# Performance work log

Measured on AMD Instinct MI355X. Metric: run time of the kernel, lower is better.

The kernel has to match this reference:

```python
import jax, jax.numpy as jnp
import numpy as np

T, N = 1024, 1024
DT = 0.5          # timestep used for velocity
DIS_THRESH = 12.0 # neighbor inclusion radius


def setup_inputs() -> dict:
    key = jax.random.key(0)
    ks = jax.random.split(key, 13)
    inp = {"a": jax.random.normal(ks[0], (T, N, 2), dtype=jnp.float32) * 10.0}
    # shared MLP (single linear layer) parameters
    inp["W1"] = jax.random.normal(ks[1], (1, 2), dtype=jnp.float32) * 0.5
    inp["b1"] = jax.random.normal(ks[2], (1,), dtype=jnp.float32) * 0.1
    inp["W2"] = jax.random.normal(ks[3], (1, 2), dtype=jnp.float32) * 0.5
    inp["b2"] = jax.random.normal(ks[4], (1,), dtype=jnp.float32) * 0.1
    inp["W3"] = jax.random.normal(ks[5], (1, 2), dtype=jnp.float32) * 0.5
    inp["b3"] = jax.random.normal(ks[6], (1,), dtype=jnp.float32) * 0.1
    inp["W4"] = jax.random.normal(ks[7], (1, 2), dtype=jnp.float32) * 0.5
    inp["b4"] = jax.random.normal(ks[8], (1,), dtype=jnp.float32) * 0.1
    inp["W5"] = jax.random.normal(ks[9], (1, 4), dtype=jnp.float32) * 0.5
    inp["b5"] = jax.random.normal(ks[10], (1,), dtype=jnp.float32) * 0.1
    inp["W6"] = jax.random.normal(ks[11], (64, 4), dtype=jnp.float32) * 0.5
    inp["b6"] = jax.random.normal(ks[12], (64,), dtype=jnp.float32) * 0.1
    return inp


def reference(a, W1, b1, W2, b2, W3, b3, W4, b4, W5, b5, W6, b6):
    # a: [T, N, 2]. Effective computation per (t in 1..T-1, node i),
    # neighbor j = N-1 (the inner qqq loop only keeps its last iteration).
    p = a[1:]              # [T-1, N, 2] current positions
    prev = a[:-1]          # [T-1, N, 2] previous positions
    pj = p[:, -1:, :]      # [T-1, 1, 2] neighbor (last node)

    dis = jnp.sqrt(jnp.sum((p - pj) ** 2, axis=-1))      # [T-1, N]
    d = p - prev                                          # displacement
    v = jnp.sqrt(jnp.sum(d ** 2, axis=-1)) / DT           # [T-1, N]
    ang = jnp.arctan2(d[..., 1], d[..., 0])               # [T-1, N]

    v_j = v[:, -1:]       # [T-1, 1]
    ang_j = ang[:, -1:]   # [T-1, 1]
    mask = (dis <= DIS_THRESH).astype(a.dtype)            # [T-1, N]

    def lin2(W, b, x0, x1):
        # 2-input linear; neighbor term masked out when dis > thresh
        return W[0, 0] * x0 + W[0, 1] * x1 + b[0]

    x_m = lin2(W1, b1, p[..., 0], mask * pj[..., 0])
    y_m = lin2(W2, b2, p[..., 1], mask * pj[..., 1])
    v_m = lin2(W3, b3, v, mask * v_j)
    a_m = lin2(W4, b4, ang, mask * ang_j)

    feat = jnp.stack([x_m, y_m, v_m, a_m], axis=-1)       # [T-1, N, 4]
    sss = jnp.einsum('tnf,of->tno', feat, W5) + b5        # [T-1, N, 1]
    sss64 = jnp.einsum('tnf,of->tno', feat, W6) + b6      # [T-1, N, 64]

    # node_out = [node[0]] + node : duplicate first computed timestep
    out1 = jnp.concatenate([sss[:1], sss], axis=0)        # [T, N, 1]
    out64 = jnp.concatenate([sss64[:1], sss64], axis=0)   # [T, N, 64]
    return out1, out64
```

## Files before the change

### kernel.cpp

```cpp
#include <hip/hip_runtime.h>

#define TT 1024
#define NN 1024
#define TS (TT - 1)
#define RPB 8
#define BT 512

typedef float v4f __attribute__((ext_vector_type(4)));

__global__ __launch_bounds__(BT) void fused_traj_kernel(
    const float* __restrict__ a,
    const float* __restrict__ W1, const float* __restrict__ b1,
    const float* __restrict__ W2, const float* __restrict__ b2,
    const float* __restrict__ W3, const float* __restrict__ b3,
    const float* __restrict__ W4, const float* __restrict__ b4,
    const float* __restrict__ W5, const float* __restrict__ b5,
    const float* __restrict__ W6, const float* __restrict__ b6,
    float* __restrict__ out1, float* __restrict__ out64)
{
    __shared__ float sFeat[RPB][64 * 4];

    const int bid    = blockIdx.x;
    const int tchunk = bid >> 4;
    const int n0     = (bid & 15) << 6;
    const int tid    = threadIdx.x;
    const int ts0    = tchunk * RPB;
    const int rows   = min(RPB, TS - ts0);

    const int wv   = tid >> 6;
    const int lane = tid & 63;

    if (wv < rows) {
        const int ts = ts0 + wv;
        const int n  = n0 + lane;
        const float2* a2 = (const float2*)a;
        const float2 p   = a2[(size_t)(ts + 1) * NN + n];
        const float2 pr  = a2[(size_t)ts * NN + n];
        const float2 pj  = a2[(size_t)(ts + 1) * NN + (NN - 1)];
        const float2 prj = a2[(size_t)ts * NN + (NN - 1)];

        const float dx  = p.x - pj.x, dy = p.y - pj.y;
        const float dis = sqrtf(dx * dx + dy * dy);

        const float ddx = p.x - pr.x, ddy = p.y - pr.y;
        const float v   = sqrtf(ddx * ddx + ddy * ddy) * 2.0f;
        const float ang = atan2f(ddy, ddx);

        const float jdx = pj.x - prj.x, jdy = pj.y - prj.y;
        const float vj   = sqrtf(jdx * jdx + jdy * jdy) * 2.0f;
        const float angj = atan2f(jdy, jdx);

        const float mask = (dis <= 12.0f) ? 1.0f : 0.0f;

        const float x_m = W1[0] * p.x + W1[1] * (mask * pj.x) + b1[0];
        const float y_m = W2[0] * p.y + W2[1] * (mask * pj.y) + b2[0];
        const float v_m = W3[0] * v   + W3[1] * (mask * vj)   + b3[0];
        const float a_m = W4[0] * ang + W4[1] * (mask * angj) + b4[0];

        const float sss = W5[0] * x_m + W5[1] * y_m + W5[2] * v_m +
                          W5[3] * a_m + b5[0];

        __builtin_nontemporal_store(sss, &out1[(size_t)(ts + 1) * NN + n]);
        if (tchunk == 0 && wv == 0)
            __builtin_nontemporal_store(sss, &out1[n]);

        sFeat[wv][lane * 4 + 0] = x_m;
        sFeat[wv][lane * 4 + 1] = y_m;
        sFeat[wv][lane * 4 + 2] = v_m;
        sFeat[wv][lane * 4 + 3] = a_m;
    }

    const int c0 = (tid & 15) * 4;
    float4 w6r[4];
    float  b6r[4];
#pragma unroll
    for (int k = 0; k < 4; ++k) {
        w6r[k] = ((const float4*)W6)[c0 + k];
        b6r[k] = b6[c0 + k];
    }

    __syncthreads();

    const int ahalf = tid >> 4;
    float* base = out64 + ((size_t)(ts0 + 1) * NN + n0) * 64;

#pragma unroll
    for (int it = 0; it < 16; ++it) {
        const int r = it >> 1;
        if (r >= rows) break;
        const int agent = ahalf + 32 * (it & 1);
        const float4 ft = ((const float4*)sFeat[r])[agent];

        v4f o;
        o.x = ft.x * w6r[0].x + ft.y * w6r[0].y + ft.z * w6r[0].z + ft.w * w6r[0].w + b6r[0];
        o.y = ft.x * w6r[1].x + ft.y * w6r[1].y + ft.z * w6r[1].z + ft.w * w6r[1].w + b6r[1];
        o.z = ft.x * w6r[2].x + ft.y * w6r[2].y + ft.z * w6r[2].z + ft.w * w6r[2].w + b6r[2];
        o.w = ft.x * w6r[3].x + ft.y * w6r[3].y + ft.z * w6r[3].z + ft.w * w6r[3].w + b6r[3];

        const size_t f = (size_t)r * (NN * 64) + agent * 64 + c0;
        __builtin_nontemporal_store(o, (v4f*)(base + f));
        if (tchunk == 0 && r == 0)
            __builtin_nontemporal_store(o, (v4f*)(out64 + (size_t)n0 * 64 + agent * 64 + c0));
    }
}

extern "C" void kernel_launch(void* const* d_in, const int* in_sizes, int n_in,
                              void* d_out, int out_size, void* d_ws, size_t ws_size,
                              hipStream_t stream)
{
    const float* a  = (const float*)d_in[0];
    const float* W1 = (const float*)d_in[1];
    const float* b1 = (const float*)d_in[2];
    const float* W2 = (const float*)d_in[3];
    const float* b2 = (const float*)d_in[4];
    const float* W3 = (const float*)d_in[5];
    const float* b3 = (const float*)d_in[6];
    const float* W4 = (const float*)d_in[7];
    const float* b4 = (const float*)d_in[8];
    const float* W5 = (const float*)d_in[9];
    const float* b5 = (const float*)d_in[10];
    const float* W6 = (const float*)d_in[11];
    const float* b6 = (const float*)d_in[12];

    float* out1  = (float*)d_out;
    float* out64 = out1 + (size_t)TT * NN;

    const int chunks = (TS + RPB - 1) / RPB;
    const int grid   = chunks * (NN / 64);
    fused_traj_kernel<<<grid, BT, 0, stream>>>(
        a, W1, b1, W2, b2, W3, b3, W4, b4, W5, b5, W6, b6, out1, out64);
}
```

Baseline: 57.04 us.

## Make each wave self-contained to replace block barrier with wave barrier

Each wave now computes features for its own 64 agents at one timestep and writes that same slice of the 64-wide output, so the block-wide __syncthreads becomes a wave-level barrier. Blocks shrink to 256 threads (4 waves, each an independent unit), and the grid covers every timestep/chunk pair exactly, so the row-count guards and early break go away. This removes cross-wave synchronisation stalls and tail handling. In exchange it launches more, smaller blocks and relies on wave-local LDS ordering being correct under a wave barrier.

After: 57.01 us. About the same (-0.1%).

```diff
diff --git a/kernel.cpp b/kernel.cpp
--- a/kernel.cpp
+++ b/kernel.cpp
@@ -3,8 +3,7 @@
 #define TT 1024
 #define NN 1024
 #define TS (TT - 1)
-#define RPB 8
-#define BT 512
+#define BT 256
 
 typedef float v4f __attribute__((ext_vector_type(4)));
 
@@ -18,59 +17,56 @@
     const float* __restrict__ W6, const float* __restrict__ b6,
     float* __restrict__ out1, float* __restrict__ out64)
 {
-    __shared__ float sFeat[RPB][64 * 4];
+    __shared__ float sFeat[4][64 * 4];
 
-    const int bid    = blockIdx.x;
-    const int tchunk = bid >> 4;
-    const int n0     = (bid & 15) << 6;
-    const int tid    = threadIdx.x;
-    const int ts0    = tchunk * RPB;
-    const int rows   = min(RPB, TS - ts0);
-
+    const int tid  = threadIdx.x;
     const int wv   = tid >> 6;
     const int lane = tid & 63;
 
-    if (wv < rows) {
-        const int ts = ts0 + wv;
-        const int n  = n0 + lane;
-        const float2* a2 = (const float2*)a;
-        const float2 p   = a2[(size_t)(ts + 1) * NN + n];
-        const float2 pr  = a2[(size_t)ts * NN + n];
-        const float2 pj  = a2[(size_t)(ts + 1) * NN + (NN - 1)];
-        const float2 prj = a2[(size_t)ts * NN + (NN - 1)];
+    const int u     = blockIdx.x * 4 + wv;
+    const int ts    = u >> 4;
+    const int chunk = u & 15;
+    const int n     = chunk * 64 + lane;
 
-        const float dx  = p.x - pj.x, dy = p.y - pj.y;
-        const float dis = sqrtf(dx * dx + dy * dy);
+    const float2* a2 = (const float2*)a;
 
-        const float ddx = p.x - pr.x, ddy = p.y - pr.y;
-        const float v   = sqrtf(ddx * ddx + ddy * ddy) * 2.0f;
-        const float ang = atan2f(ddy, ddx);
+    const float2 p   = a2[(size_t)(ts + 1) * NN + n];
+    const float2 pr  = a2[(size_t)ts * NN + n];
+    const float2 pj  = a2[(size_t)(ts + 1) * NN + (NN - 1)];
+    const float2 prj = a2[(size_t)ts * NN + (NN - 1)];
 
-        const float jdx = pj.x - prj.x, jdy = pj.y - prj.y;
-        const float vj   = sqrtf(jdx * jdx + jdy * jdy) * 2.0f;
-        const float angj = atan2f(jdy, jdx);
+    const float dx  = p.x - pj.x, dy = p.y - pj.y;
+    const float dis = sqrtf(dx * dx + dy * dy);
 
-        const float mask = (dis <= 12.0f) ? 1.0f : 0.0f;
+    const float ddx = p.x - pr.x, ddy = p.y - pr.y;
+    const float v   = sqrtf(ddx * ddx + ddy * ddy) * 2.0f;
+    const float ang = atan2f(ddy, ddx);
 
-        const float x_m = W1[0] * p.x + W1[1] * (mask * pj.x) + b1[0];
-        const float y_m = W2[0] * p.y + W2[1] * (mask * pj.y) + b2[0];
-        const float v_m = W3[0] * v   + W3[1] * (mask * vj)   + b3[0];
-        const float a_m = W4[0] * ang + W4[1] * (mask * angj) + b4[0];
+    const float jdx = pj.x - prj.x, jdy = pj.y - prj.y;
+    const float vj   = sqrtf(jdx * jdx + jdy * jdy) * 2.0f;
+    const float angj = atan2f(jdy, jdx);
 
-        const float sss = W5[0] * x_m + W5[1] * y_m + W5[2] * v_m +
-                          W5[3] * a_m + b5[0];
+    const float mask = (dis <= 12.0f) ? 1.0f : 0.0f;
 
-        __builtin_nontemporal_store(sss, &out1[(size_t)(ts + 1) * NN + n]);
-        if (tchunk == 0 && wv == 0)
-            __builtin_nontemporal_store(sss, &out1[n]);
+    const float x_m = W1[0] * p.x + W1[1] * (mask * pj.x) + b1[0];
+    const float y_m = W2[0] * p.y + W2[1] * (mask * pj.y) + b2[0];
+    const float v_m = W3[0] * v   + W3[1] * (mask * vj)   + b3[0];
+    const float a_m = W4[0] * ang + W4[1] * (mask * angj) + b4[0];
 
-        sFeat[wv][lane * 4 + 0] = x_m;
-        sFeat[wv][lane * 4 + 1] = y_m;
-        sFeat[wv][lane * 4 + 2] = v_m;
-        sFeat[wv][lane * 4 + 3] = a_m;
-    }
+    const float sss = W5[0] * x_m + W5[1] * y_m + W5[2] * v_m +
+                      W5[3] * a_m + b5[0];
 
-    const int c0 = (tid & 15) * 4;
+    __builtin_nontemporal_store(sss, &out1[(size_t)(ts + 1) * NN + n]);
+    if (ts == 0)
+        __builtin_nontemporal_store(sss, &out1[n]);
+
+    float* myFeat = sFeat[wv];
+    myFeat[lane * 4 + 0] = x_m;
+    myFeat[lane * 4 + 1] = y_m;
+    myFeat[lane * 4 + 2] = v_m;
+    myFeat[lane * 4 + 3] = a_m;
+
+    const int c0 = (lane & 15) * 4;
     float4 w6r[4];
     float  b6r[4];
 #pragma unroll
@@ -79,17 +75,15 @@
         b6r[k] = b6[c0 + k];
     }
 
-    __syncthreads();
+    __builtin_amdgcn_wave_barrier();
 
-    const int ahalf = tid >> 4;
-    float* base = out64 + ((size_t)(ts0 + 1) * NN + n0) * 64;
+    float* dst  = out64 + ((size_t)(ts + 1) * NN + chunk * 64) * 64 + lane * 4;
+    float* dst0 = out64 + ((size_t)chunk * 64) * 64 + lane * 4;
 
 #pragma unroll
     for (int it = 0; it < 16; ++it) {
-        const int r = it >> 1;
-        if (r >= rows) break;
-        const int agent = ahalf + 32 * (it & 1);
-        const float4 ft = ((const float4*)sFeat[r])[agent];
+        const int al = (lane >> 4) + 4 * it;
+        const float4 ft = ((const float4*)myFeat)[al];
 
         v4f o;
         o.x = ft.x * w6r[0].x + ft.y * w6r[0].y + ft.z * w6r[0].z + ft.w * w6r[0].w + b6r[0];
@@ -97,10 +91,9 @@
         o.z = ft.x * w6r[2].x + ft.y * w6r[2].y + ft.z * w6r[2].z + ft.w * w6r[2].w + b6r[2];
         o.w = ft.x * w6r[3].x + ft.y * w6r[3].y + ft.z * w6r[3].z + ft.w * w6r[3].w + b6r[3];
 
-        const size_t f = (size_t)r * (NN * 64) + agent * 64 + c0;
-        __builtin_nontemporal_store(o, (v4f*)(base + f));
-        if (tchunk == 0 && r == 0)
-            __builtin_nontemporal_store(o, (v4f*)(out64 + (size_t)n0 * 64 + agent * 64 + c0));
+        __builtin_nontemporal_store(o, (v4f*)(dst + it * 256));
+        if (ts == 0)
+            __builtin_nontemporal_store(o, (v4f*)(dst0 + it * 256));
     }
 }
 
@@ -125,8 +118,7 @@
     float* out1  = (float*)d_out;
     float* out64 = out1 + (size_t)TT * NN;
 
-    const int chunks = (TS + RPB - 1) / RPB;
-    const int grid   = chunks * (NN / 64);
+    const int grid = (TS * 16) / 4;
     fused_traj_kernel<<<grid, BT, 0, stream>>>(
         a, W1, b1, W2, b2, W3, b3, W4, b4, W5, b5, W6, b6, out1, out64);
 }
```
